# Kernel tuning notes

Measured on AMD Instinct MI355X. Metric: run time of the kernel, lower is better.

## Reference

```python
import jax, jax.numpy as jnp
import numpy as np

H = 64; W = 64; WS = 8; SS = 4; NH = 8; C = 256; IM = 4


def _rel_pos_index(ws: int) -> np.ndarray:
    coords = np.stack(np.meshgrid(np.arange(ws), np.arange(ws), indexing='ij'), axis=0).reshape(2, -1)
    rel = (coords[:, :, None] - coords[:, None, :]).transpose(1, 2, 0)
    rel[:, :, 0] += ws - 1
    rel[:, :, 1] += ws - 1
    rel[:, :, 0] *= 2 * ws - 1
    return rel.sum(-1).astype(np.int64)  # (ws*ws, ws*ws)


def _shift_mask(h: int, w: int, ws: int, ss: int) -> np.ndarray:
    img = np.zeros((h, w), np.float32)
    sl = (slice(0, -ws), slice(-ws, -ss), slice(-ss, None))
    cnt = 0
    for hs in sl:
        for wsl in sl:
            img[hs, wsl] = cnt
            cnt += 1
    mw = img.reshape(h // ws, ws, w // ws, ws).transpose(0, 2, 1, 3).reshape(-1, ws * ws)
    am = mw[:, None, :] - mw[:, :, None]
    return np.where(am != 0, -100.0, 0.0).astype(np.float32)  # (nW, n, n)


def setup_inputs() -> dict:
    key = jax.random.key(0)
    ks = jax.random.split(key, 16)
    s = 0.02
    d_ff = C * IM
    n_rel = (2 * WS - 1) ** 2
    return {
        'hidden_states': jax.random.normal(ks[0], (32, H * W, C), jnp.float32),
        'ln1_g': jnp.ones((C,), jnp.float32),
        'ln1_b': jnp.zeros((C,), jnp.float32),
        'wq': jax.random.normal(ks[1], (C, C), jnp.float32) * s,
        'bq': jnp.zeros((C,), jnp.float32),
        'wk': jax.random.normal(ks[2], (C, C), jnp.float32) * s,
        'bk': jnp.zeros((C,), jnp.float32),
        'wv': jax.random.normal(ks[3], (C, C), jnp.float32) * s,
        'bv': jnp.zeros((C,), jnp.float32),
        'bias_table': jax.random.normal(ks[4], (n_rel, NH), jnp.float32) * s,
        'wo': jax.random.normal(ks[5], (C, C), jnp.float32) * s,
        'bo': jnp.zeros((C,), jnp.float32),
        'ln2_g': jnp.ones((C,), jnp.float32),
        'ln2_b': jnp.zeros((C,), jnp.float32),
        'w1': jax.random.normal(ks[6], (C, d_ff), jnp.float32) * s,
        'b1': jnp.zeros((d_ff,), jnp.float32),
        'w2': jax.random.normal(ks[7], (d_ff, C), jnp.float32) * s,
        'b2': jnp.zeros((C,), jnp.float32),
    }


def _layernorm(x, g, b):
    m = x.mean(-1, keepdims=True)
    v = ((x - m) ** 2).mean(-1, keepdims=True)
    return (x - m) * jax.lax.rsqrt(v + 1e-5) * g + b


def reference(hidden_states, ln1_g, ln1_b, wq, bq, wk, bk, wv, bv, bias_table,
              wo, bo, ln2_g, ln2_b, w1, b1, w2, b2):
    B = hidden_states.shape[0]
    n = WS * WS
    hd = C // NH
    scale = hd ** -0.5
    nhw, nww = H // WS, W // WS
    nW = nhw * nww
    rpi = jnp.asarray(_rel_pos_index(WS))        # (n, n) int
    mask = jnp.asarray(_shift_mask(H, W, WS, SS))  # (nW, n, n)

    shortcut = hidden_states
    x = _layernorm(hidden_states, ln1_g, ln1_b).reshape(B, H, W, C)
    # cyclic shift
    x = jnp.roll(x, (-SS, -SS), axis=(1, 2))
    # window partition -> (B*nW, n, C)
    x = x.reshape(B, nhw, WS, nww, WS, C).transpose(0, 1, 3, 2, 4, 5).reshape(B * nW, n, C)

    q = (x @ wq + bq).reshape(B * nW, n, NH, hd).transpose(0, 2, 1, 3)
    k = (x @ wk + bk).reshape(B * nW, n, NH, hd).transpose(0, 2, 1, 3)
    v = (x @ wv + bv).reshape(B * nW, n, NH, hd).transpose(0, 2, 1, 3)

    attn = jnp.einsum('whnd,whmd->whnm', q, k) * scale  # (B*nW, NH, n, n)
    bias = bias_table[rpi.reshape(-1)].reshape(n, n, NH).transpose(2, 0, 1)
    attn = attn + bias[None]
    attn = attn.reshape(B, nW, NH, n, n) + mask[None, :, None]
    attn = jax.nn.softmax(attn.reshape(B * nW, NH, n, n), axis=-1)

    out = jnp.einsum('whnm,whmd->whnd', attn, v).transpose(0, 2, 1, 3).reshape(B * nW, n, C)
    out = out @ wo + bo
    # window reverse
    out = out.reshape(B, nhw, nww, WS, WS, C).transpose(0, 1, 3, 2, 4, 5).reshape(B, H, W, C)
    out = jnp.roll(out, (SS, SS), axis=(1, 2)).reshape(B, H * W, C)

    hs = shortcut + out
    y = _layernorm(hs, ln2_g, ln2_b)
    y = jax.nn.gelu(y @ w1 + b1, approximate=False)
    y = y @ w2 + b2
    return hs + y
```

## Files before the change

### kernel.cpp

```cpp
#include <hip/hip_runtime.h>
#include <hip/hip_bf16.h>
#include <math.h>

typedef unsigned short u16;
typedef __attribute__((ext_vector_type(8))) short bf16x8;
typedef __attribute__((ext_vector_type(8))) unsigned short u16x8;
typedef __attribute__((ext_vector_type(4))) float f32x4;

#define MFMA_BF16 __builtin_amdgcn_mfma_f32_16x16x32_bf16

__device__ __forceinline__ u16 f2bf(float f){
  union { float f; unsigned u; } v; v.f = f;
  unsigned r = v.u + 0x7FFFu + ((v.u >> 16) & 1u);
  return (u16)(r >> 16);
}

__device__ __forceinline__ void gll16(const void* g, void* l){
  __builtin_amdgcn_global_load_lds(
      (const __attribute__((address_space(1))) unsigned int*)g,
      (__attribute__((address_space(3))) unsigned int*)l, 16, 0, 0);
}

__global__ void k_concat_bias(const float* __restrict__ a, const float* __restrict__ b,
                              const float* __restrict__ c, float* __restrict__ o){
  int i = threadIdx.x;
  o[i] = i < 256 ? a[i] : (i < 512 ? b[i-256] : c[i-512]);
}

__global__ __launch_bounds__(256) void k_wfrag(const float* __restrict__ W, u16* __restrict__ F,
                                               int K, int N){
  int idx = blockIdx.x*256 + threadIdx.x;
  int nks = K >> 5;
  int per_n16 = nks << 9;
  int n16 = idx / per_n16; int rem = idx - n16*per_n16;
  int ks = rem >> 9, l8 = rem & 511, lane = l8 >> 3, j = l8 & 7;
  int k = ks*32 + ((lane >> 4) << 3) + j;
  int n = (n16 << 4) + (lane & 15);
  F[idx] = f2bf(W[(size_t)k*N + n]);
}

__global__ __launch_bounds__(256) void k_fragw(const float* __restrict__ wq, const float* __restrict__ wk,
                                               const float* __restrict__ wv, u16* __restrict__ fragW){
  int idx = blockIdx.x*256 + threadIdx.x;
  int j = idx & 7, lane = (idx >> 3) & 63, nj = (idx >> 9) & 1;
  int ks = (idx >> 10) & 7, h = (idx >> 13) & 7, type = idx >> 16;
  const float* w = type == 0 ? wq : (type == 1 ? wk : wv);
  int k = ks*32 + 8*(lane >> 4) + j;
  int n = h*32 + nj*16 + (lane & 15);
  fragW[idx] = f2bf(w[(size_t)k*256 + n]);
}

__global__ __launch_bounds__(256) void k_bias(const float* __restrict__ btab, float* __restrict__ fb){
  int idx = blockIdx.x*256 + threadIdx.x;
  int nj = idx & 3, lr = (idx >> 2) & 15, m = (idx >> 6) & 63, hh = (idx >> 12) & 7, cls = idx >> 15;
  int n = nj*16 + lr;
  int r1=m>>3, c1=m&7, r2=n>>3, c2=n&7;
  float bv = btab[((r1-r2+7)*15 + (c1-c2+7))*8 + hh];
  int whe = cls>>1, wwe = cls&1;
  int a1 = (whe ? (r1<4?1:2) : 0)*3 + (wwe ? (c1<4?1:2) : 0);
  int a2 = (whe ? (r2<4?1:2) : 0)*3 + (wwe ? (c2<4?1:2) : 0);
  fb[idx] = bv + ((a1!=a2) ? -100.f : 0.f);
}

__global__ __launch_bounds__(1024) void k_fattn(const float* __restrict__ hidden,
    const float* __restrict__ g1, const float* __restrict__ b1f,
    const u16* __restrict__ fragW, const float* __restrict__ bqkv,
    const float* __restrict__ fb, const u16* __restrict__ woF,
    const float* __restrict__ bo, const float* __restrict__ g2,
    const float* __restrict__ b2v,
    float* __restrict__ hs_out, u16* __restrict__ y2)
{
  __shared__ __align__(16) u16 lds[75776];
  int tid = threadIdx.x, lane = tid & 63, wid = tid >> 6;
  int lg = lane >> 4, lr = lane & 15;
  int h = wid >> 1, s = wid & 1;
  int gw = blockIdx.x;
  int bi = gw >> 6, win = gw & 63, wh = win >> 3, wwi = win & 7;

  {
    int t = wid*4 + (lane >> 4);
    int j = lane & 15;
    int hh_ = (wh*8 + (t >> 3) + 4) & 63;
    int ww_ = (wwi*8 + (t & 7) + 4) & 63;
    const float4* row = (const float4*)(hidden + ((size_t)bi*4096 + hh_*64 + ww_)*256) + j*4;
    float4 v[4]; float sm = 0.f, sq = 0.f;
#pragma unroll
    for (int i=0;i<4;i++){
      v[i] = row[i];
      sm += v[i].x+v[i].y+v[i].z+v[i].w;
      sq += v[i].x*v[i].x+v[i].y*v[i].y+v[i].z*v[i].z+v[i].w*v[i].w;
    }
    sm += __shfl_xor(sm,1); sq += __shfl_xor(sq,1);
    sm += __shfl_xor(sm,2); sq += __shfl_xor(sq,2);
    sm += __shfl_xor(sm,4); sq += __shfl_xor(sq,4);
    sm += __shfl_xor(sm,8); sq += __shfl_xor(sq,8);
    float mean = sm*(1.f/256.f);
    float inv = rsqrtf(sq*(1.f/256.f) - mean*mean + 1e-5f);
    const float4* gg = (const float4*)g1 + j*4;
    const float4* bb = (const float4*)b1f + j*4;
#pragma unroll
    for (int i2=0;i2<2;i2++){
      float4 a0=v[2*i2], a1=v[2*i2+1];
      float4 g0=gg[2*i2], g1_=gg[2*i2+1];
      float4 b0=bb[2*i2], b1_=bb[2*i2+1];
      u16x8 pk;
      pk[0]=f2bf((a0.x-mean)*inv*g0.x+b0.x); pk[1]=f2bf((a0.y-mean)*inv*g0.y+b0.y);
      pk[2]=f2bf((a0.z-mean)*inv*g0.z+b0.z); pk[3]=f2bf((a0.w-mean)*inv*g0.w+b0.w);
      pk[4]=f2bf((a1.x-mean)*inv*g1_.x+b1_.x); pk[5]=f2bf((a1.y-mean)*inv*g1_.y+b1_.y);
      pk[6]=f2bf((a1.z-mean)*inv*g1_.z+b1_.z); pk[7]=f2bf((a1.w-mean)*inv*g1_.w+b1_.w);
      int c = (j*2 + i2) ^ (t & 7);
      *(u16x8*)(&lds[t*256 + c*8]) = pk;
    }
  }
  __syncthreads();

  f32x4 qa[2][2]={}, ka[2][2]={}, va[2][2]={};
  __builtin_amdgcn_s_setprio(1);
#pragma unroll
  for (int ks=0; ks<8; ks++){
    bf16x8 af[2];
#pragma unroll
    for (int mi=0;mi<2;mi++){
      int tok = 32*s + mi*16 + lr;
      af[mi] = *(const bf16x8*)(&lds[tok*256 + (((ks*4+lg) ^ (tok&7))*8)]);
    }
    const u16* fq = fragW + ((((size_t)h)*8 + ks)*2)*512 + lane*8;
#pragma unroll
    for (int nj=0;nj<2;nj++){
      bf16x8 bq_ = *(const bf16x8*)(fq + nj*512);
      bf16x8 bk_ = *(const bf16x8*)(fq + 65536 + nj*512);
      bf16x8 bv_ = *(const bf16x8*)(fq + 131072 + nj*512);
#pragma unroll
      for (int mi=0;mi<2;mi++){
        qa[mi][nj] = MFMA_BF16(af[mi], bq_, qa[mi][nj], 0,0,0);
        ka[mi][nj] = MFMA_BF16(af[mi], bk_, ka[mi][nj], 0,0,0);
        va[mi][nj] = MFMA_BF16(af[mi], bv_, va[mi][nj], 0,0,0);
      }
    }
  }
  __builtin_amdgcn_s_setprio(0);

  u16* hb  = &lds[16384 + h*7424];
  u16* k_h = hb;
  u16* v_h = hb + 2560;
  u16* q_s = hb + 4864 + s*1280;
  const float scale = 0.1767766952966369f;
#pragma unroll
  for (int mi=0;mi<2;mi++)
#pragma unroll
  for (int nj=0;nj<2;nj++){
    int dim = nj*16+lr;
    float bq_ = bqkv[h*32+dim], bk_ = bqkv[256+h*32+dim], bv_ = bqkv[512+h*32+dim];
#pragma unroll
    for (int r=0;r<4;r++){
      int tokl = mi*16+4*lg+r;
      q_s[tokl*40+dim] = f2bf((qa[mi][nj][r]+bq_)*scale);
      k_h[(32*s+tokl)*40+dim] = f2bf(ka[mi][nj][r]+bk_);
    }
    ushort4 vp;
    vp.x = f2bf(va[mi][nj][0]+bv_); vp.y = f2bf(va[mi][nj][1]+bv_);
    vp.z = f2bf(va[mi][nj][2]+bv_); vp.w = f2bf(va[mi][nj][3]+bv_);
    *(ushort4*)(&v_h[dim*72 + 32*s + mi*16 + 4*lg]) = vp;
  }
  __syncthreads();

  bf16x8 qf[2], kf[4];
#pragma unroll
  for (int i=0;i<2;i++)
    qf[i] = *(const bf16x8*)(&q_s[(i*16+lr)*40 + 8*lg]);
#pragma unroll
  for (int i=0;i<4;i++)
    kf[i] = *(const bf16x8*)(&k_h[(i*16+lr)*40 + 8*lg]);
  f32x4 acc[2][4] = {};
#pragma unroll
  for (int mi=0;mi<2;mi++)
#pragma unroll
  for (int nj=0;nj<4;nj++)
    acc[mi][nj] = MFMA_BF16(qf[mi], kf[nj], acc[mi][nj], 0,0,0);

  int cls = ((wh==7) ? 2 : 0) | ((wwi==7) ? 1 : 0);
  const float4* fb4 = (const float4*)(fb + (((size_t)cls*8 + h) << 12));
#pragma unroll
  for (int mi=0;mi<2;mi++)
#pragma unroll
  for (int r=0;r<4;r++){
    int m = 32*s + mi*16 + 4*lg + r;
    float4 bv4 = fb4[m*16 + lr];
#pragma unroll
    for (int nj=0;nj<4;nj++)
      acc[mi][nj][r] += bv4[nj];
  }
#pragma unroll
  for (int mi=0;mi<2;mi++)
#pragma unroll
  for (int r=0;r<4;r++){
    float mx = fmaxf(fmaxf(acc[mi][0][r], acc[mi][1][r]), fmaxf(acc[mi][2][r], acc[mi][3][r]));
    for (int off=1; off<16; off<<=1) mx = fmaxf(mx, __shfl_xor(mx, off));
    float sum = 0.f;
#pragma unroll
    for (int nj=0;nj<4;nj++){ float e = __expf(acc[mi][nj][r]-mx); acc[mi][nj][r]=e; sum+=e; }
    for (int off=1; off<16; off<<=1) sum += __shfl_xor(sum, off);
    float inv = 1.f/sum;
#pragma unroll
    for (int nj=0;nj<4;nj++) acc[mi][nj][r] *= inv;
  }

  __syncthreads();

  u16* P_s = s ? hb : (hb + 4864);
#pragma unroll
  for (int mi=0;mi<2;mi++)
#pragma unroll
  for (int nj=0;nj<4;nj++)
#pragma unroll
  for (int r=0;r<4;r++)
    P_s[(mi*16+4*lg+r)*72 + nj*16 + lr] = f2bf(acc[mi][nj][r]);

  f32x4 acc2[2][2] = {};
#pragma unroll
  for (int ks=0; ks<2; ks++){
    bf16x8 vf0 = *(const bf16x8*)(&v_h[(lr)*72 + ks*32 + 8*lg]);
    bf16x8 vf1 = *(const bf16x8*)(&v_h[(16+lr)*72 + ks*32 + 8*lg]);
#pragma unroll
    for (int mi=0;mi<2;mi++){
      bf16x8 pf = *(const bf16x8*)(&P_s[(mi*16+lr)*72 + ks*32 + 8*lg]);
      acc2[mi][0] = MFMA_BF16(pf, vf0, acc2[mi][0], 0,0,0);
      acc2[mi][1] = MFMA_BF16(pf, vf1, acc2[mi][1], 0,0,0);
    }
  }

#pragma unroll
  for (int mi=0;mi<2;mi++)
#pragma unroll
  for (int nt=0;nt<2;nt++)
#pragma unroll
  for (int r=0;r<4;r++){
    int row = 32*s + mi*16 + 4*lg + r;
    int chunk = (4*h + 2*nt + (lr>>3)) ^ (row & 7);
    lds[row*256 + chunk*8 + (lr&7)] = f2bf(acc2[mi][nt][r]);
  }
  __syncthreads();

  f32x4 po[2][2] = {};
  __builtin_amdgcn_s_setprio(1);
#pragma unroll
  for (int ks=0; ks<8; ks++){
    bf16x8 af2[2];
#pragma unroll
    for (int mi=0;mi<2;mi++){
      int row = 32*s + mi*16 + lr;
      af2[mi] = *(const bf16x8*)(&lds[row*256 + (((ks*4+lg) ^ (row&7))*8)]);
    }
#pragma unroll
    for (int nj=0;nj<2;nj++){
      bf16x8 bw = *(const bf16x8*)(woF + (((size_t)(2*h+nj))*8 + ks)*512 + lane*8);
#pragma unroll
      for (int mi=0;mi<2;mi++)
        po[mi][nj] = MFMA_BF16(af2[mi], bw, po[mi][nj], 0,0,0);
    }
  }
  __builtin_amdgcn_s_setprio(0);

  float* part_s = (float*)&lds[16384];
  float* part_q = (float*)&lds[16384 + 1024];
  float bov[2], g2v[2], b2vv[2];
#pragma unroll
  for (int nj=0;nj<2;nj++){
    int n = 32*h + nj*16 + lr;
    bov[nj] = bo[n]; g2v[nj] = g2[n]; b2vv[nj] = b2v[n];
  }
#pragma unroll
  for (int mi=0;mi<2;mi++)
#pragma unroll
  for (int r=0;r<4;r++){
    int p = 32*s + mi*16 + 4*lg + r;
    int hh_ = (wh*8 + (p >> 3) + 4) & 63;
    int ww_ = (wwi*8 + (p & 7) + 4) & 63;
    size_t base = ((size_t)bi*4096 + hh_*64 + ww_)*256;
    float ls = 0.f, lq = 0.f;
#pragma unroll
    for (int nj=0;nj<2;nj++){
      int n = 32*h + nj*16 + lr;
      float v = po[mi][nj][r] + bov[nj] + hidden[base + n];
      hs_out[base + n] = v;
      po[mi][nj][r] = v;
      ls += v; lq += v*v;
    }
    ls += __shfl_xor(ls,1); lq += __shfl_xor(lq,1);
    ls += __shfl_xor(ls,2); lq += __shfl_xor(lq,2);
    ls += __shfl_xor(ls,4); lq += __shfl_xor(lq,4);
    ls += __shfl_xor(ls,8); lq += __shfl_xor(lq,8);
    if (lr == 0){ part_s[p*8 + h] = ls; part_q[p*8 + h] = lq; }
  }
  __syncthreads();

#pragma unroll
  for (int mi=0;mi<2;mi++)
#pragma unroll
  for (int r=0;r<4;r++){
    int p = 32*s + mi*16 + 4*lg + r;
    int hh_ = (wh*8 + (p >> 3) + 4) & 63;
    int ww_ = (wwi*8 + (p & 7) + 4) & 63;
    size_t base = ((size_t)bi*4096 + hh_*64 + ww_)*256;
    float sum = 0.f, sqq = 0.f;
#pragma unroll
    for (int hh2=0; hh2<8; hh2++){ sum += part_s[p*8 + hh2]; sqq += part_q[p*8 + hh2]; }
    float mean = sum*(1.f/256.f);
    float inv = rsqrtf(sqq*(1.f/256.f) - mean*mean + 1e-5f);
#pragma unroll
    for (int nj=0;nj<2;nj++){
      int n = 32*h + nj*16 + lr;
      y2[base + n] = f2bf((po[mi][nj][r]-mean)*inv*g2v[nj] + b2vv[nj]);
    }
  }
}

#define GSTAGE_A(buf, k0)                                                \
  _Pragma("unroll")                                                      \
  for (int c = 0; c < 4; c++){                                           \
    int row = c*64 + srow;                                               \
    gll16(Aw + (size_t)row*K + (k0) + (scb>>1), &As[buf][c*4096 + tid*8]); \
  }

#define BLOAD(t)                                                         \
  _Pragma("unroll")                                                      \
  for (int kk = 0; kk < 2; kk++){                                        \
    int ks = ((t)<<1) + kk;                                              \
    _Pragma("unroll")                                                    \
    for (int j = 0; j < 4; j++)                                          \
      bfr[kk][j] = *(const bf16x8*)(WF + ((((size_t)(nb16 + wc*4 + j))*nks + ks)<<9) + lane*8); \
  }

#define GLOOP_BODY(b)                                                    \
  _Pragma("unroll")                                                      \
  for (int kk = 0; kk < 2; kk++){                                        \
    int cbr = (kk*64 + 16*g) ^ ((lr & 7) << 4);                          \
    bf16x8 af[8];                                                        \
    _Pragma("unroll")                                                    \
    for (int i=0;i<8;i++)                                                \
      af[i] = *(const bf16x8*)(&As[b][(wr*128 + i*16 + lr)*64 + (cbr>>1)]); \
    _Pragma("unroll")                                                    \
    for (int mi=0;mi<8;mi++)                                             \
    _Pragma("unroll")                                                    \
    for (int nj=0;nj<4;nj++)                                             \
      acc[mi][nj] = MFMA_BF16(af[mi], bfr[kk][nj], acc[mi][nj], 0,0,0);  \
  }

#define GLOOP(nt)                                                        \
  GSTAGE_A(0, 0)                                                         \
  GSTAGE_A(1, 64)                                                        \
  BLOAD(0)                                                               \
  for (int t = 0; t < (nt); t++){                                        \
    if (t+1 < (nt)) asm volatile("s_waitcnt vmcnt(12)" ::: "memory");    \
    else            asm volatile("s_waitcnt vmcnt(8)" ::: "memory");     \
    __builtin_amdgcn_s_barrier();                                        \
    __builtin_amdgcn_sched_barrier(0);                                   \
    int b = t & 1;                                                       \
    GLOOP_BODY(b)                                                        \
    __builtin_amdgcn_sched_barrier(0);                                   \
    asm volatile("s_waitcnt lgkmcnt(0)" ::: "memory");                   \
    __builtin_amdgcn_s_barrier();                                        \
    __builtin_amdgcn_sched_barrier(0);                                   \
    if (t+1 < (nt)){ BLOAD(t+1) }                                        \
    if (t+2 < (nt)){ GSTAGE_A(b, (t+2)<<6) }                             \
  }

template<int EPI, bool SWZ>
__global__ __launch_bounds__(512, 2) void k_gemm256(const u16* __restrict__ A, const u16* __restrict__ WF,
                                                    const float* __restrict__ bias, const float* __restrict__ res,
                                                    void* __restrict__ outp, int K){
  __shared__ __align__(16) u16 As[2][16384];
  int tid = threadIdx.x, lane = tid & 63, wid = tid >> 6;
  int g = lane >> 4, lr = lane & 15;
  int wr = wid >> 2, wc = wid & 3;
  int bx, by;
  if constexpr (SWZ){
    int nwg = gridDim.x*gridDim.y;
    int bid = blockIdx.y*gridDim.x + blockIdx.x;
    int cpx = nwg >> 3;
    int swz = (bid & 7)*cpx + (bid >> 3);
    bx = swz % gridDim.x; by = swz / gridDim.x;
  } else { bx = blockIdx.x; by = blockIdx.y; }
  int m0 = by*256, n0 = bx*256;
  int nb16 = bx << 4;
  int nks = K >> 5;
  const u16* Aw = A + (size_t)m0*K;
  int srow = tid >> 3;
  int scb  = ((tid & 7)*16) ^ ((srow & 7) << 4);
  f32x4 acc[8][4] = {};
  bf16x8 bfr[2][4];
  int nt = K >> 6;

  GLOOP(nt)

#pragma unroll
  for (int mi=0; mi<8; mi++)
#pragma unroll
  for (int nj=0; nj<4; nj++){
    int n = n0 + wc*64 + nj*16 + lr;
#pragma unroll
    for (int r=0; r<4; r++){
      int m = m0 + wr*128 + mi*16 + 4*g + r;
      float val = acc[mi][nj][r] + bias[n];
      if constexpr (EPI==2){
        float gv = 0.5f*val*(1.f + erff(val*0.70710678118654752f));
        ((u16*)outp)[(size_t)m*1024 + n] = f2bf(gv);
      } else {
        ((float*)outp)[(size_t)m*256 + n] = val + res[(size_t)m*256 + n];
      }
    }
  }
}

extern "C" void kernel_launch(void* const* d_in, const int* in_sizes, int n_in,
                              void* d_out, int out_size, void* d_ws, size_t ws_size,
                              hipStream_t stream){
  const float* hidden = (const float*)d_in[0];
  const float* ln1g = (const float*)d_in[1];
  const float* ln1b = (const float*)d_in[2];
  const float* wq   = (const float*)d_in[3];
  const float* bq   = (const float*)d_in[4];
  const float* wk   = (const float*)d_in[5];
  const float* bk   = (const float*)d_in[6];
  const float* wv   = (const float*)d_in[7];
  const float* bv   = (const float*)d_in[8];
  const float* btab = (const float*)d_in[9];
  const float* wo   = (const float*)d_in[10];
  const float* bo   = (const float*)d_in[11];
  const float* ln2g = (const float*)d_in[12];
  const float* ln2b = (const float*)d_in[13];
  const float* w1   = (const float*)d_in[14];
  const float* b1   = (const float*)d_in[15];
  const float* w2   = (const float*)d_in[16];
  const float* b2   = (const float*)d_in[17];
  float* out = (float*)d_out;

  char* ws = (char*)d_ws;
  const size_t MB = 1ull << 20;
  u16* y1c   = (u16*)(ws + 64*MB);
  u16* y2ln  = (u16*)(ws + 192*MB);
  u16* fragW = (u16*)(ws + 256*MB);
  u16* woF   = fragW + 196608;
  u16* w1F   = woF + 65536;
  u16* w2F   = w1F + 262144;
  float* bqkv = (float*)(w2F + 262144);
  float* fbias = bqkv + 1024;

  k_fragw<<<768, 256, 0, stream>>>(wq, wk, wv, fragW);
  k_wfrag<<<256, 256, 0, stream>>>(wo, woF, 256, 256);
  k_wfrag<<<1024,256, 0, stream>>>(w1, w1F, 256, 1024);
  k_wfrag<<<1024,256, 0, stream>>>(w2, w2F, 1024, 256);
  k_concat_bias<<<1, 768, 0, stream>>>(bq, bk, bv, bqkv);
  k_bias<<<512, 256, 0, stream>>>(btab, fbias);

  k_fattn<<<2048, 1024, 0, stream>>>(hidden, ln1g, ln1b, fragW, bqkv, fbias,
                                     woF, bo, ln2g, ln2b, out, y2ln);
  for (int mc = 0; mc < 2; mc++){
    k_gemm256<2,true><<<dim3(4, 256), 512, 0, stream>>>(y2ln + (size_t)mc*65536*256, w1F, b1, nullptr, y1c, 256);
    k_gemm256<3,false><<<dim3(1, 256), 512, 0, stream>>>(y1c, w2F, b2,
                                                         out + (size_t)mc*65536*256,
                                                         out + (size_t)mc*65536*256, 1024);
  }
}
```

Measured before the change: 559.3 us.

## Fuse MLP fc1+GELU+fc2 into one kernel keeping hidden activations in LDS

Replaces the two-GEMM MLP (fc1 with GELU writing a bf16 intermediate to global, then fc2 with residual add) with a single kernel. Each 64-row block holds its LayerNorm output in LDS and processes the 1024-wide hidden dimension in four chunks of 256, keeping each GELU chunk in LDS and accumulating fc2 immediately. This removes the round trip of the large intermediate through global memory and the separate launches. In exchange it uses a small 64-row tile, loads B weights straight from global without staging, and adds barriers per chunk, so MFMA efficiency and weight reuse may drop.

```diff
diff --git a/kernel.cpp b/kernel.cpp
--- a/kernel.cpp
+++ b/kernel.cpp
@@ -315,100 +315,101 @@
   }
 }
 
-#define GSTAGE_A(buf, k0)                                                \
-  _Pragma("unroll")                                                      \
-  for (int c = 0; c < 4; c++){                                           \
-    int row = c*64 + srow;                                               \
-    gll16(Aw + (size_t)row*K + (k0) + (scb>>1), &As[buf][c*4096 + tid*8]); \
-  }
-
-#define BLOAD(t)                                                         \
-  _Pragma("unroll")                                                      \
-  for (int kk = 0; kk < 2; kk++){                                        \
-    int ks = ((t)<<1) + kk;                                              \
-    _Pragma("unroll")                                                    \
-    for (int j = 0; j < 4; j++)                                          \
-      bfr[kk][j] = *(const bf16x8*)(WF + ((((size_t)(nb16 + wc*4 + j))*nks + ks)<<9) + lane*8); \
-  }
-
-#define GLOOP_BODY(b)                                                    \
-  _Pragma("unroll")                                                      \
-  for (int kk = 0; kk < 2; kk++){                                        \
-    int cbr = (kk*64 + 16*g) ^ ((lr & 7) << 4);                          \
-    bf16x8 af[8];                                                        \
-    _Pragma("unroll")                                                    \
-    for (int i=0;i<8;i++)                                                \
-      af[i] = *(const bf16x8*)(&As[b][(wr*128 + i*16 + lr)*64 + (cbr>>1)]); \
-    _Pragma("unroll")                                                    \
-    for (int mi=0;mi<8;mi++)                                             \
-    _Pragma("unroll")                                                    \
-    for (int nj=0;nj<4;nj++)                                             \
-      acc[mi][nj] = MFMA_BF16(af[mi], bfr[kk][nj], acc[mi][nj], 0,0,0);  \
-  }
-
-#define GLOOP(nt)                                                        \
-  GSTAGE_A(0, 0)                                                         \
-  GSTAGE_A(1, 64)                                                        \
-  BLOAD(0)                                                               \
-  for (int t = 0; t < (nt); t++){                                        \
-    if (t+1 < (nt)) asm volatile("s_waitcnt vmcnt(12)" ::: "memory");    \
-    else            asm volatile("s_waitcnt vmcnt(8)" ::: "memory");     \
-    __builtin_amdgcn_s_barrier();                                        \
-    __builtin_amdgcn_sched_barrier(0);                                   \
-    int b = t & 1;                                                       \
-    GLOOP_BODY(b)                                                        \
-    __builtin_amdgcn_sched_barrier(0);                                   \
-    asm volatile("s_waitcnt lgkmcnt(0)" ::: "memory");                   \
-    __builtin_amdgcn_s_barrier();                                        \
-    __builtin_amdgcn_sched_barrier(0);                                   \
-    if (t+1 < (nt)){ BLOAD(t+1) }                                        \
-    if (t+2 < (nt)){ GSTAGE_A(b, (t+2)<<6) }                             \
-  }
-
-template<int EPI, bool SWZ>
-__global__ __launch_bounds__(512, 2) void k_gemm256(const u16* __restrict__ A, const u16* __restrict__ WF,
-                                                    const float* __restrict__ bias, const float* __restrict__ res,
-                                                    void* __restrict__ outp, int K){
-  __shared__ __align__(16) u16 As[2][16384];
+__global__ __launch_bounds__(512) void k_mlp(const u16* __restrict__ y2ln,
+    const u16* __restrict__ w1F, const u16* __restrict__ w2F,
+    const float* __restrict__ b1, const float* __restrict__ b2,
+    float* __restrict__ io)
+{
+  __shared__ __align__(16) u16 lds[32768];
   int tid = threadIdx.x, lane = tid & 63, wid = tid >> 6;
-  int g = lane >> 4, lr = lane & 15;
-  int wr = wid >> 2, wc = wid & 3;
-  int bx, by;
-  if constexpr (SWZ){
-    int nwg = gridDim.x*gridDim.y;
-    int bid = blockIdx.y*gridDim.x + blockIdx.x;
-    int cpx = nwg >> 3;
-    int swz = (bid & 7)*cpx + (bid >> 3);
-    bx = swz % gridDim.x; by = swz / gridDim.x;
-  } else { bx = blockIdx.x; by = blockIdx.y; }
-  int m0 = by*256, n0 = bx*256;
-  int nb16 = bx << 4;
-  int nks = K >> 5;
-  const u16* Aw = A + (size_t)m0*K;
-  int srow = tid >> 3;
-  int scb  = ((tid & 7)*16) ^ ((srow & 7) << 4);
-  f32x4 acc[8][4] = {};
-  bf16x8 bfr[2][4];
-  int nt = K >> 6;
-
-  GLOOP(nt)
-
-#pragma unroll
-  for (int mi=0; mi<8; mi++)
-#pragma unroll
-  for (int nj=0; nj<4; nj++){
-    int n = n0 + wc*64 + nj*16 + lr;
-#pragma unroll
-    for (int r=0; r<4; r++){
-      int m = m0 + wr*128 + mi*16 + 4*g + r;
-      float val = acc[mi][nj][r] + bias[n];
-      if constexpr (EPI==2){
-        float gv = 0.5f*val*(1.f + erff(val*0.70710678118654752f));
-        ((u16*)outp)[(size_t)m*1024 + n] = f2bf(gv);
-      } else {
-        ((float*)outp)[(size_t)m*256 + n] = val + res[(size_t)m*256 + n];
-      }
-    }
+  int lg = lane >> 4, lr = lane & 15;
+  int wr_ = wid >> 2, wc_ = wid & 3;
+  int m0 = blockIdx.x*64;
+
+  {
+    int row_lo = tid >> 5;
+    int ch = tid & 31;
+#pragma unroll
+    for (int i=0;i<4;i++){
+      int row = i*16 + row_lo;
+      int sch = ch ^ (row & 7);
+      gll16(y2ln + (size_t)(m0+row)*256 + sch*8, &lds[i*4096 + tid*8]);
+    }
+  }
+  asm volatile("s_waitcnt vmcnt(0)" ::: "memory");
+  __syncthreads();
+
+  u16* xt = &lds[16384];
+  f32x4 accY[2][4] = {};
+  float b2v[4];
+#pragma unroll
+  for (int nj=0;nj<4;nj++) b2v[nj] = b2[wc_*64 + nj*16 + lr];
+
+  for (int c = 0; c < 4; c++){
+    f32x4 acc1[4][2] = {};
+    __builtin_amdgcn_s_setprio(1);
+#pragma unroll
+    for (int ks=0; ks<8; ks++){
+      bf16x8 af[4];
+#pragma unroll
+      for (int mi=0;mi<4;mi++){
+        int row = mi*16 + lr;
+        af[mi] = *(const bf16x8*)(&lds[row*256 + (((ks*4+lg) ^ (row&7))<<3)]);
+      }
+#pragma unroll
+      for (int nj=0;nj<2;nj++){
+        bf16x8 bw = *(const bf16x8*)(w1F + ((((size_t)(c*16 + wid*2 + nj))*8 + ks)<<9) + lane*8);
+#pragma unroll
+        for (int mi=0;mi<4;mi++)
+          acc1[mi][nj] = MFMA_BF16(af[mi], bw, acc1[mi][nj], 0,0,0);
+      }
+    }
+    __builtin_amdgcn_s_setprio(0);
+    __syncthreads();
+#pragma unroll
+    for (int mi=0;mi<4;mi++)
+#pragma unroll
+    for (int nj=0;nj<2;nj++){
+      float b1v = b1[c*256 + wid*32 + nj*16 + lr];
+#pragma unroll
+      for (int r=0;r<4;r++){
+        int row = mi*16 + 4*lg + r;
+        int col = wid*32 + nj*16 + lr;
+        float v = acc1[mi][nj][r] + b1v;
+        v = 0.5f*v*(1.f + erff(v*0.70710678118654752f));
+        xt[row*256 + ((((col>>3) ^ (row&7))<<3) | (col&7))] = f2bf(v);
+      }
+    }
+    __syncthreads();
+    __builtin_amdgcn_s_setprio(1);
+#pragma unroll
+    for (int ks=0; ks<8; ks++){
+      bf16x8 af2[2];
+#pragma unroll
+      for (int mi=0;mi<2;mi++){
+        int row = wr_*32 + mi*16 + lr;
+        af2[mi] = *(const bf16x8*)(&xt[row*256 + (((ks*4+lg) ^ (row&7))<<3)]);
+      }
+#pragma unroll
+      for (int nj=0;nj<4;nj++){
+        bf16x8 bw = *(const bf16x8*)(w2F + ((((size_t)(wc_*4 + nj))*32 + c*8 + ks)<<9) + lane*8);
+#pragma unroll
+        for (int mi=0;mi<2;mi++)
+          accY[mi][nj] = MFMA_BF16(af2[mi], bw, accY[mi][nj], 0,0,0);
+      }
+    }
+    __builtin_amdgcn_s_setprio(0);
+  }
+
+#pragma unroll
+  for (int mi=0;mi<2;mi++)
+#pragma unroll
+  for (int nj=0;nj<4;nj++)
+#pragma unroll
+  for (int r=0;r<4;r++){
+    int m = m0 + wr_*32 + mi*16 + 4*lg + r;
+    int n = wc_*64 + nj*16 + lr;
+    io[(size_t)m*256 + n] = accY[mi][nj][r] + b2v[nj] + io[(size_t)m*256 + n];
   }
 }
 
@@ -437,7 +438,6 @@
 
   char* ws = (char*)d_ws;
   const size_t MB = 1ull << 20;
-  u16* y1c   = (u16*)(ws + 64*MB);
   u16* y2ln  = (u16*)(ws + 192*MB);
   u16* fragW = (u16*)(ws + 256*MB);
   u16* woF   = fragW + 196608;
@@ -455,10 +455,5 @@
 
   k_fattn<<<2048, 1024, 0, stream>>>(hidden, ln1g, ln1b, fragW, bqkv, fbias,
                                      woF, bo, ln2g, ln2b, out, y2ln);
-  for (int mc = 0; mc < 2; mc++){
-    k_gemm256<2,true><<<dim3(4, 256), 512, 0, stream>>>(y2ln + (size_t)mc*65536*256, w1F, b1, nullptr, y1c, 256);
-    k_gemm256<3,false><<<dim3(1, 256), 512, 0, stream>>>(y1c, w2F, b2,
-                                                         out + (size_t)mc*65536*256,
-                                                         out + (size_t)mc*65536*256, 1024);
-  }
-}
+  k_mlp<<<2048, 512, 0, stream>>>(y2ln, w1F, w2F, b1, b2, out);
+}
```

Measured after the change: 536.6 us. 1.04x faster.
